# Kernel tuning notes

Hardware: AMD Instinct MI355X
Metric: run time of the kernel (lower is better)

The kernel has to match this reference:

```python
import jax, jax.numpy as jnp
import numpy as np

D_MODEL = 768
N_HEADS = 12
D_FF = 3072
D_K = D_MODEL // N_HEADS


def _layernorm(x, gamma, beta, eps=1e-5):
    mu = jnp.mean(x, axis=-1, keepdims=True)
    var = jnp.var(x, axis=-1, keepdims=True)
    return (x - mu) * jax.lax.rsqrt(var + eps) * gamma + beta


def setup_inputs() -> dict:
    key = jax.random.key(0)
    ks = jax.random.split(key, 16)
    B, S = 2, 2048
    s = 1.0 / np.sqrt(D_MODEL)
    inp = {
        "x": jax.random.normal(ks[0], (B, S, D_MODEL), jnp.float32),
        "mask": jnp.ones((B, 1, 1, S), jnp.int32),
        "wq": jax.random.normal(ks[1], (D_MODEL, D_MODEL), jnp.float32) * s,
        "bq": jnp.zeros((D_MODEL,), jnp.float32),
        "wk": jax.random.normal(ks[2], (D_MODEL, D_MODEL), jnp.float32) * s,
        "bk": jnp.zeros((D_MODEL,), jnp.float32),
        "wv": jax.random.normal(ks[3], (D_MODEL, D_MODEL), jnp.float32) * s,
        "bv": jnp.zeros((D_MODEL,), jnp.float32),
        "wo": jax.random.normal(ks[4], (D_MODEL, D_MODEL), jnp.float32) * s,
        "bo": jnp.zeros((D_MODEL,), jnp.float32),
        "w1": jax.random.normal(ks[5], (D_MODEL, D_FF), jnp.float32) * s,
        "b1": jnp.zeros((D_FF,), jnp.float32),
        "w2": jax.random.normal(ks[6], (D_FF, D_MODEL), jnp.float32) / np.sqrt(D_FF),
        "b2": jnp.zeros((D_MODEL,), jnp.float32),
        "g1": jnp.ones((D_MODEL,), jnp.float32),
        "be1": jnp.zeros((D_MODEL,), jnp.float32),
        "g2": jnp.ones((D_MODEL,), jnp.float32),
        "be2": jnp.zeros((D_MODEL,), jnp.float32),
    }
    return inp


def reference(x, mask, wq, bq, wk, bk, wv, bv, wo, bo, w1, b1, w2, b2, g1, be1, g2, be2):
    B, S, _ = x.shape
    # QKV projections, split into heads: [B, H, S, d_k]
    q = (x @ wq + bq).reshape(B, S, N_HEADS, D_K).transpose(0, 2, 1, 3)
    k = (x @ wk + bk).reshape(B, S, N_HEADS, D_K).transpose(0, 2, 1, 3)
    v = (x @ wv + bv).reshape(B, S, N_HEADS, D_K).transpose(0, 2, 1, 3)
    # [B, H, S, S]
    scores = jnp.einsum('bhqd,bhkd->bhqk', q, k) / np.sqrt(D_K).astype(np.float32)
    scores = jnp.where(mask == 0, -1e9, scores)
    attn = jax.nn.softmax(scores, axis=-1)  # dropout is identity in eval
    ctx = jnp.einsum('bhqk,bhkd->bhqd', attn, v)
    ctx = ctx.transpose(0, 2, 1, 3).reshape(B, S, D_MODEL)
    attn_out = ctx @ wo + bo
    x = _layernorm(x + attn_out, g1, be1)
    ff = jax.nn.gelu(x @ w1 + b1, approximate=False) @ w2 + b2
    x = _layernorm(x + ff, g2, be2)
    return x
```

## Files before the change

### kernel.cpp

```cpp
#include <hip/hip_runtime.h>
#include <hip/hip_bf16.h>
#include <math.h>

#define D_MODEL 768
#define N_HEADS 12
#define D_FF    3072
#define D_K     64
#define SEQ     2048
#define BATCH   2
#define M_TOK   (BATCH * SEQ)
#define D_QKV   (3 * D_MODEL)
#define BH      (BATCH * N_HEADS)

typedef __attribute__((ext_vector_type(8))) short short8;
typedef __attribute__((ext_vector_type(4))) float f32x4;

static __device__ __forceinline__ short f2bf(float f) {
    __hip_bfloat16 b = __float2bfloat16(f);
    return __builtin_bit_cast(short, b);
}

static __device__ __forceinline__ void load_lds16(const void* g, void* l) {
    __builtin_amdgcn_global_load_lds(
        (const __attribute__((address_space(1))) unsigned int*)g,
        (__attribute__((address_space(3))) unsigned int*)l,
        16, 0, 0);
}

__global__ __launch_bounds__(256) void prep_kernel(
    const float* __restrict__ x,  short* __restrict__ xb,
    const float* __restrict__ wq, const float* __restrict__ wk,
    const float* __restrict__ wv, short* __restrict__ wqkv_t,
    const float* __restrict__ wo, short* __restrict__ wo_t,
    const float* __restrict__ w1, short* __restrict__ w1_t,
    const float* __restrict__ w2, short* __restrict__ w2_t,
    const float* __restrict__ bq, const float* __restrict__ bk,
    const float* __restrict__ bv, float* __restrict__ bqkv)
{
    __shared__ float tile[32][33];
    const int bid = blockIdx.x;
    const int tid = threadIdx.x;

    if (bid < 6912) {
        const float* in; short* outp; int K, N, t;
        if (bid < 576)       { in = wq; outp = wqkv_t;                 K = 768;  N = 768;  t = bid; }
        else if (bid < 1152) { in = wk; outp = wqkv_t + 589824;        K = 768;  N = 768;  t = bid - 576; }
        else if (bid < 1728) { in = wv; outp = wqkv_t + 2 * 589824;    K = 768;  N = 768;  t = bid - 1152; }
        else if (bid < 2304) { in = wo; outp = wo_t;                   K = 768;  N = 768;  t = bid - 1728; }
        else if (bid < 4608) { in = w1; outp = w1_t;                   K = 768;  N = 3072; t = bid - 2304; }
        else                 { in = w2; outp = w2_t;                   K = 3072; N = 768;  t = bid - 4608; }
        const int nb = N >> 5;
        const int bx = t % nb, by = t / nb;
        const int n0 = bx * 32, k0 = by * 32;
        const int tx = tid & 31, ty = tid >> 5;
#pragma unroll
        for (int i = 0; i < 32; i += 8)
            tile[ty + i][tx] = in[(size_t)(k0 + ty + i) * N + n0 + tx];
        __syncthreads();
#pragma unroll
        for (int i = 0; i < 32; i += 8)
            outp[(size_t)(n0 + ty + i) * K + k0 + tx] = f2bf(tile[tx][ty + i]);
    } else if (bid < 8448) {
        const int t = (bid - 6912) * 256 + tid;
        const float4 a = reinterpret_cast<const float4*>(x)[2 * t];
        const float4 b = reinterpret_cast<const float4*>(x)[2 * t + 1];
        short8 s;
        s[0] = f2bf(a.x); s[1] = f2bf(a.y); s[2] = f2bf(a.z); s[3] = f2bf(a.w);
        s[4] = f2bf(b.x); s[5] = f2bf(b.y); s[6] = f2bf(b.z); s[7] = f2bf(b.w);
        reinterpret_cast<short8*>(xb)[t] = s;
    } else {
        const int t = (bid - 8448) * 256 + tid;
        if (t < D_QKV)
            bqkv[t] = (t < 768) ? bq[t] : (t < 1536) ? bk[t - 768] : bv[t - 1536];
    }
}

#define EPI_QKV     0
#define EPI_GELU_BF 1
#define EPI_RES_F32 2

template <int EPI>
__global__ __launch_bounds__(256) void gemm_mfma(
    const short* __restrict__ A,
    const short* __restrict__ Bt,
    const float* __restrict__ bias,
    const float* __restrict__ res,
    void* __restrict__ Cout,
    void* __restrict__ Out2,
    void* __restrict__ Out3,
    int M, int N, int K)
{
    __shared__ short As[128 * 32];
    __shared__ short Bs[128 * 32];

    const int tid  = threadIdx.x;
    const int w    = tid >> 6;
    const int lane = tid & 63;
    const int m16  = lane & 15;
    const int quad = lane >> 4;
    const int wm   = w >> 1;
    const int wn   = w & 1;
    const int bm = blockIdx.y * 128;
    const int bn = blockIdx.x * 128;

    const int sr = lane >> 2;
    const int sc = (lane & 3) * 8;

    f32x4 acc[4][4];
#pragma unroll
    for (int mt = 0; mt < 4; ++mt)
#pragma unroll
        for (int nt = 0; nt < 4; ++nt)
            acc[mt][nt] = (f32x4){0.f, 0.f, 0.f, 0.f};

    for (int k0 = 0; k0 < K; k0 += 32) {
        __syncthreads();
#pragma unroll
        for (int i = 0; i < 2; ++i) {
            const int row = i * 64 + w * 16 + sr;
            load_lds16(&A [(size_t)(bm + row) * K + k0 + sc],
                       &As[i * 2048 + w * 512]);
            load_lds16(&Bt[(size_t)(bn + row) * K + k0 + sc],
                       &Bs[i * 2048 + w * 512]);
        }
        __syncthreads();

        short8 af[4], bf[4];
#pragma unroll
        for (int mt = 0; mt < 4; ++mt)
            af[mt] = *reinterpret_cast<const short8*>(
                &As[(wm * 64 + mt * 16 + m16) * 32 + quad * 8]);
#pragma unroll
        for (int nt = 0; nt < 4; ++nt)
            bf[nt] = *reinterpret_cast<const short8*>(
                &Bs[(wn * 64 + nt * 16 + m16) * 32 + quad * 8]);
#pragma unroll
        for (int mt = 0; mt < 4; ++mt)
#pragma unroll
            for (int nt = 0; nt < 4; ++nt)
                acc[mt][nt] = __builtin_amdgcn_mfma_f32_16x16x32_bf16(
                    af[mt], bf[nt], acc[mt][nt], 0, 0, 0);
    }

#pragma unroll
    for (int mt = 0; mt < 4; ++mt) {
#pragma unroll
        for (int r = 0; r < 4; ++r) {
            const int row = bm + wm * 64 + mt * 16 + quad * 4 + r;
#pragma unroll
            for (int nt = 0; nt < 4; ++nt) {
                const int col = bn + wn * 64 + nt * 16 + m16;
                float v = acc[mt][nt][r] + bias[col];
                if (EPI == EPI_QKV) {
                    const int b = row >> 11;
                    const int s = row & 2047;
                    const int sec = (col >= 1536) ? 2 : (col >= 768) ? 1 : 0;
                    const int cm = col - sec * 768;
                    const int h = cm >> 6;
                    const int d = cm & 63;
                    const int bh = b * N_HEADS + h;
                    if (sec == 0) {
                        ((short*)Cout)[((size_t)bh * SEQ + s) * 64 + d] = f2bf(v * 0.125f);
                    } else if (sec == 1) {
                        ((short*)Out2)[((size_t)bh * SEQ + s) * 64 + d] = f2bf(v);
                    } else {
                        ((short*)Out3)[((size_t)bh * 64 + d) * SEQ + s] = f2bf(v);
                    }
                } else if (EPI == EPI_GELU_BF) {
                    v = 0.5f * v * (1.0f + erff(v * 0.70710678118654752f));
                    ((short*)Cout)[(size_t)row * N + col] = f2bf(v);
                } else {
                    v += res[(size_t)row * N + col];
                    ((float*)Cout)[(size_t)row * N + col] = v;
                }
            }
        }
    }
}

template <int EPI>
__global__ __launch_bounds__(256) void gemm_bn64(
    const short* __restrict__ A, const short* __restrict__ Bt,
    const float* __restrict__ bias, const float* __restrict__ res,
    void* __restrict__ Cout, int M, int N, int K)
{
    __shared__ short As[128 * 32];
    __shared__ short Bs[64 * 32];

    const int tid  = threadIdx.x;
    const int w    = tid >> 6;
    const int lane = tid & 63;
    const int m16  = lane & 15;
    const int quad = lane >> 4;
    const int bm = blockIdx.y * 128;
    const int bn = blockIdx.x * 64;

    const int sr = lane >> 2;
    const int sc = (lane & 3) * 8;

    f32x4 acc[2][4];
#pragma unroll
    for (int mt = 0; mt < 2; ++mt)
#pragma unroll
        for (int nt = 0; nt < 4; ++nt)
            acc[mt][nt] = (f32x4){0.f, 0.f, 0.f, 0.f};

    for (int k0 = 0; k0 < K; k0 += 32) {
        __syncthreads();
#pragma unroll
        for (int i = 0; i < 2; ++i) {
            const int row = i * 64 + w * 16 + sr;
            load_lds16(&A[(size_t)(bm + row) * K + k0 + sc],
                       &As[i * 2048 + w * 512]);
        }
        load_lds16(&Bt[(size_t)(bn + w * 16 + sr) * K + k0 + sc], &Bs[w * 512]);
        __syncthreads();

        short8 af[2], bf[4];
#pragma unroll
        for (int mt = 0; mt < 2; ++mt)
            af[mt] = *reinterpret_cast<const short8*>(
                &As[(w * 32 + mt * 16 + m16) * 32 + quad * 8]);
#pragma unroll
        for (int nt = 0; nt < 4; ++nt)
            bf[nt] = *reinterpret_cast<const short8*>(
                &Bs[(nt * 16 + m16) * 32 + quad * 8]);
#pragma unroll
        for (int mt = 0; mt < 2; ++mt)
#pragma unroll
            for (int nt = 0; nt < 4; ++nt)
                acc[mt][nt] = __builtin_amdgcn_mfma_f32_16x16x32_bf16(
                    af[mt], bf[nt], acc[mt][nt], 0, 0, 0);
    }

#pragma unroll
    for (int mt = 0; mt < 2; ++mt) {
#pragma unroll
        for (int r = 0; r < 4; ++r) {
            const int row = bm + w * 32 + mt * 16 + quad * 4 + r;
#pragma unroll
            for (int nt = 0; nt < 4; ++nt) {
                const int col = bn + nt * 16 + m16;
                float v = acc[mt][nt][r] + bias[col];
                if (EPI == EPI_RES_F32) {
                    v += res[(size_t)row * N + col];
                    ((float*)Cout)[(size_t)row * N + col] = v;
                } else {
                    ((short*)Cout)[(size_t)row * N + col] = f2bf(v);
                }
            }
        }
    }
}

#define KT 64
#define LDS_STR 72

__global__ __launch_bounds__(256) void attn_mfma_kernel(
    const short* __restrict__ qb, const short* __restrict__ kb,
    const short* __restrict__ vtb, const int* __restrict__ mask,
    short* __restrict__ ctx)
{
    __shared__ short Klds[KT * LDS_STR];
    __shared__ short Vtlds[D_K * LDS_STR];
    __shared__ short Plds[4 * 16 * LDS_STR];

    const int tid  = threadIdx.x;
    const int lane = tid & 63;
    const int wv   = tid >> 6;
    const int m16  = lane & 15;
    const int quad = lane >> 4;

    const int qtile = blockIdx.x * 64;
    const int bh = blockIdx.y;
    const int b = bh / N_HEADS;

    const size_t qrow = (size_t)bh * SEQ + qtile + wv * 16 + m16;
    short8 qf[2];
#pragma unroll
    for (int kc = 0; kc < 2; ++kc)
        qf[kc] = *reinterpret_cast<const short8*>(
            &qb[qrow * 64 + kc * 32 + quad * 8]);

    short8 ones;
#pragma unroll
    for (int i = 0; i < 8; ++i) ones[i] = (short)0x3F80;

    f32x4 o[4];
#pragma unroll
    for (int nt = 0; nt < 4; ++nt) o[nt] = (f32x4){0.f, 0.f, 0.f, 0.f};
    f32x4 lacc = (f32x4){0.f, 0.f, 0.f, 0.f};

    const int* mrow = mask + (size_t)b * SEQ;

    for (int kt0 = 0; kt0 < SEQ; kt0 += KT) {
        __syncthreads();

        {
            const int key = tid >> 2;
            const int dg = (tid & 3) * 16;
            const short* src = &kb[((size_t)bh * SEQ + kt0 + key) * 64 + dg];
            *reinterpret_cast<short8*>(&Klds[key * LDS_STR + dg]) =
                *reinterpret_cast<const short8*>(src);
            *reinterpret_cast<short8*>(&Klds[key * LDS_STR + dg + 8]) =
                *reinterpret_cast<const short8*>(src + 8);
        }
        {
            const int d = tid >> 2;
            const int kg = (tid & 3) * 16;
            const short* src = &vtb[((size_t)bh * 64 + d) * SEQ + kt0 + kg];
            *reinterpret_cast<short8*>(&Vtlds[d * LDS_STR + kg]) =
                *reinterpret_cast<const short8*>(src);
            *reinterpret_cast<short8*>(&Vtlds[d * LDS_STR + kg + 8]) =
                *reinterpret_cast<const short8*>(src + 8);
        }
        __syncthreads();

        f32x4 s[4];
#pragma unroll
        for (int nt = 0; nt < 4; ++nt) s[nt] = (f32x4){0.f, 0.f, 0.f, 0.f};
#pragma unroll
        for (int nt = 0; nt < 4; ++nt) {
#pragma unroll
            for (int kc = 0; kc < 2; ++kc) {
                const short8 kf = *reinterpret_cast<const short8*>(
                    &Klds[(nt * 16 + m16) * LDS_STR + kc * 32 + quad * 8]);
                s[nt] = __builtin_amdgcn_mfma_f32_16x16x32_bf16(qf[kc], kf, s[nt], 0, 0, 0);
            }
        }

        short* Pw = &Plds[wv * 16 * LDS_STR];
#pragma unroll
        for (int nt = 0; nt < 4; ++nt) {
            const int mk = mrow[kt0 + nt * 16 + m16];
#pragma unroll
            for (int r = 0; r < 4; ++r) {
                const float sv = (mk == 0) ? -1e9f : fminf(s[nt][r], 30.f);
                Pw[(quad * 4 + r) * LDS_STR + nt * 16 + m16] = f2bf(__expf(sv));
            }
        }

#pragma unroll
        for (int kc = 0; kc < 2; ++kc) {
            const short8 af = *reinterpret_cast<const short8*>(
                &Pw[m16 * LDS_STR + kc * 32 + quad * 8]);
#pragma unroll
            for (int nt = 0; nt < 4; ++nt) {
                const short8 bf = *reinterpret_cast<const short8*>(
                    &Vtlds[(nt * 16 + m16) * LDS_STR + kc * 32 + quad * 8]);
                o[nt] = __builtin_amdgcn_mfma_f32_16x16x32_bf16(af, bf, o[nt], 0, 0, 0);
            }
            lacc = __builtin_amdgcn_mfma_f32_16x16x32_bf16(af, ones, lacc, 0, 0, 0);
        }
    }

    const int h = bh % N_HEADS;
#pragma unroll
    for (int r = 0; r < 4; ++r) {
        const float inv_l = 1.0f / lacc[r];
        const size_t row = (size_t)(b * SEQ + qtile + wv * 16 + quad * 4 + r);
#pragma unroll
        for (int nt = 0; nt < 4; ++nt)
            ctx[row * D_MODEL + h * D_K + nt * 16 + m16] = f2bf(o[nt][r] * inv_l);
    }
}

template <bool DUAL>
__global__ __launch_bounds__(256) void layernorm_kernel(
    const float* __restrict__ in, const float* __restrict__ g,
    const float* __restrict__ be, float* __restrict__ outf,
    short* __restrict__ outb)
{
    const int row = blockIdx.x;
    const float* x = in + (size_t)row * D_MODEL;

    float s = 0.0f, s2 = 0.0f;
    for (int i = threadIdx.x; i < D_MODEL; i += 256) {
        const float v = x[i];
        s += v; s2 += v * v;
    }
#pragma unroll
    for (int off = 32; off > 0; off >>= 1) {
        s  += __shfl_down(s, off);
        s2 += __shfl_down(s2, off);
    }
    __shared__ float red[2][4];
    const int wid = threadIdx.x >> 6;
    const int lane = threadIdx.x & 63;
    if (lane == 0) { red[0][wid] = s; red[1][wid] = s2; }
    __syncthreads();
    __shared__ float stats[2];
    if (threadIdx.x == 0) {
        float ts = 0.0f, ts2 = 0.0f;
#pragma unroll
        for (int w = 0; w < 4; ++w) { ts += red[0][w]; ts2 += red[1][w]; }
        const float mu = ts * (1.0f / D_MODEL);
        const float var = ts2 * (1.0f / D_MODEL) - mu * mu;
        stats[0] = mu;
        stats[1] = rsqrtf(var + 1e-5f);
    }
    __syncthreads();
    const float mu = stats[0], rstd = stats[1];
    for (int i = threadIdx.x; i < D_MODEL; i += 256) {
        const float v = (x[i] - mu) * rstd * g[i] + be[i];
        outf[(size_t)row * D_MODEL + i] = v;
        if (DUAL) outb[(size_t)row * D_MODEL + i] = f2bf(v);
    }
}

extern "C" void kernel_launch(void* const* d_in, const int* in_sizes, int n_in,
                              void* d_out, int out_size, void* d_ws, size_t ws_size,
                              hipStream_t stream)
{
    const float* x    = (const float*)d_in[0];
    const int*   mask = (const int*)  d_in[1];
    const float* wq   = (const float*)d_in[2];
    const float* bq   = (const float*)d_in[3];
    const float* wk   = (const float*)d_in[4];
    const float* bk   = (const float*)d_in[5];
    const float* wv   = (const float*)d_in[6];
    const float* bv   = (const float*)d_in[7];
    const float* wo   = (const float*)d_in[8];
    const float* bo   = (const float*)d_in[9];
    const float* w1   = (const float*)d_in[10];
    const float* b1   = (const float*)d_in[11];
    const float* w2   = (const float*)d_in[12];
    const float* b2   = (const float*)d_in[13];
    const float* g1   = (const float*)d_in[14];
    const float* be1  = (const float*)d_in[15];
    const float* g2   = (const float*)d_in[16];
    const float* be2  = (const float*)d_in[17];

    float* out = (float*)d_out;

    char* cur = (char*)d_ws;
    auto alloc = [&](size_t bytes) { char* p = cur; cur += (bytes + 255) & ~(size_t)255; return p; };

    short* xb      = (short*)alloc((size_t)M_TOK * D_MODEL * 2);
    short* qbuf    = (short*)alloc((size_t)BH * SEQ * D_K * 2);
    short* kbuf    = (short*)alloc((size_t)BH * SEQ * D_K * 2);
    short* vtbuf   = (short*)alloc((size_t)BH * D_K * SEQ * 2);
    short* ctxb    = (short*)alloc((size_t)M_TOK * D_MODEL * 2);
    short* x1b     = (short*)alloc((size_t)M_TOK * D_MODEL * 2);
    short* ffb     = (short*)alloc((size_t)M_TOK * D_FF * 2);
    short* wqkv_t  = (short*)alloc((size_t)D_QKV * D_MODEL * 2);
    short* wo_t    = (short*)alloc((size_t)D_MODEL * D_MODEL * 2);
    short* w1_t    = (short*)alloc((size_t)D_FF * D_MODEL * 2);
    short* w2_t    = (short*)alloc((size_t)D_MODEL * D_FF * 2);
    float* bqkv    = (float*)alloc((size_t)D_QKV * 4);
    float* h1      = (float*)alloc((size_t)M_TOK * D_MODEL * 4);
    float* x1f     = (float*)alloc((size_t)M_TOK * D_MODEL * 4);
    float* h2      = (float*)alloc((size_t)M_TOK * D_MODEL * 4);

    const dim3 blk(256);

    hipLaunchKernelGGL(prep_kernel, dim3(8457), blk, 0, stream,
                       x, xb, wq, wk, wv, wqkv_t, wo, wo_t,
                       w1, w1_t, w2, w2_t, bq, bk, bv, bqkv);

    hipLaunchKernelGGL((gemm_mfma<EPI_QKV>), dim3(D_QKV / 128, M_TOK / 128), blk, 0, stream,
                       xb, wqkv_t, bqkv, nullptr, qbuf, kbuf, vtbuf, M_TOK, D_QKV, D_MODEL);

    hipLaunchKernelGGL(attn_mfma_kernel, dim3(SEQ / 64, BH), blk, 0, stream,
                       qbuf, kbuf, vtbuf, mask, ctxb);

    hipLaunchKernelGGL((gemm_bn64<EPI_RES_F32>), dim3(D_MODEL / 64, M_TOK / 128), blk, 0, stream,
                       ctxb, wo_t, bo, x, h1, M_TOK, D_MODEL, D_MODEL);

    hipLaunchKernelGGL((layernorm_kernel<true>), dim3(M_TOK), blk, 0, stream,
                       h1, g1, be1, x1f, x1b);

    hipLaunchKernelGGL((gemm_mfma<EPI_GELU_BF>), dim3(D_FF / 128, M_TOK / 128), blk, 0, stream,
                       x1b, w1_t, b1, nullptr, ffb, nullptr, nullptr, M_TOK, D_FF, D_MODEL);

    hipLaunchKernelGGL((gemm_bn64<EPI_RES_F32>), dim3(D_MODEL / 64, M_TOK / 128), blk, 0, stream,
                       ffb, w2_t, b2, x1f, h2, M_TOK, D_MODEL, D_FF);

    hipLaunchKernelGGL((layernorm_kernel<false>), dim3(M_TOK), blk, 0, stream,
                       h2, g2, be2, out, nullptr);
}
```

Before: 371.3 us.

## Deepen GEMM K-tile to 64 with XOR-swizzled LDS, widen attention key tile, approximate GELU

```diff
diff --git a/kernel.cpp b/kernel.cpp
--- a/kernel.cpp
+++ b/kernel.cpp
@@ -20,6 +20,13 @@
     return __builtin_bit_cast(short, b);
 }
 
+static __device__ __forceinline__ float gelu_f(float v) {
+    const float u = 0.7978845608f * (v + 0.044715f * v * v * v);
+    const float e = __expf(2.0f * u);
+    const float t = 1.0f - 2.0f / (e + 1.0f);
+    return 0.5f * v * (1.0f + t);
+}
+
 static __device__ __forceinline__ void load_lds16(const void* g, void* l) {
     __builtin_amdgcn_global_load_lds(
         (const __attribute__((address_space(1))) unsigned int*)g,
@@ -43,12 +50,12 @@
 
     if (bid < 6912) {
         const float* in; short* outp; int K, N, t;
-        if (bid < 576)       { in = wq; outp = wqkv_t;                 K = 768;  N = 768;  t = bid; }
-        else if (bid < 1152) { in = wk; outp = wqkv_t + 589824;        K = 768;  N = 768;  t = bid - 576; }
-        else if (bid < 1728) { in = wv; outp = wqkv_t + 2 * 589824;    K = 768;  N = 768;  t = bid - 1152; }
-        else if (bid < 2304) { in = wo; outp = wo_t;                   K = 768;  N = 768;  t = bid - 1728; }
-        else if (bid < 4608) { in = w1; outp = w1_t;                   K = 768;  N = 3072; t = bid - 2304; }
-        else                 { in = w2; outp = w2_t;                   K = 3072; N = 768;  t = bid - 4608; }
+        if (bid < 576)       { in = wq; outp = wqkv_t;              K = 768;  N = 768;  t = bid; }
+        else if (bid < 1152) { in = wk; outp = wqkv_t + 589824;     K = 768;  N = 768;  t = bid - 576; }
+        else if (bid < 1728) { in = wv; outp = wqkv_t + 2 * 589824; K = 768;  N = 768;  t = bid - 1152; }
+        else if (bid < 2304) { in = wo; outp = wo_t;                K = 768;  N = 768;  t = bid - 1728; }
+        else if (bid < 4608) { in = w1; outp = w1_t;                K = 768;  N = 3072; t = bid - 2304; }
+        else                 { in = w2; outp = w2_t;                K = 3072; N = 768;  t = bid - 4608; }
         const int nb = N >> 5;
         const int bx = t % nb, by = t / nb;
         const int n0 = bx * 32, k0 = by * 32;
@@ -85,13 +92,11 @@
     const short* __restrict__ Bt,
     const float* __restrict__ bias,
     const float* __restrict__ res,
-    void* __restrict__ Cout,
-    void* __restrict__ Out2,
-    void* __restrict__ Out3,
+    void* __restrict__ Cout, void* __restrict__ Out2, void* __restrict__ Out3,
     int M, int N, int K)
 {
-    __shared__ short As[128 * 32];
-    __shared__ short Bs[128 * 32];
+    __shared__ short As[128 * 64];
+    __shared__ short Bs[128 * 64];
 
     const int tid  = threadIdx.x;
     const int w    = tid >> 6;
@@ -103,8 +108,9 @@
     const int bm = blockIdx.y * 128;
     const int bn = blockIdx.x * 128;
 
-    const int sr = lane >> 2;
-    const int sc = (lane & 3) * 8;
+    const int l8 = lane >> 3;
+    const int scol = ((lane & 7) ^ l8) * 8;
+    const int rx = m16 & 7;
 
     f32x4 acc[4][4];
 #pragma unroll
@@ -113,33 +119,36 @@
         for (int nt = 0; nt < 4; ++nt)
             acc[mt][nt] = (f32x4){0.f, 0.f, 0.f, 0.f};
 
-    for (int k0 = 0; k0 < K; k0 += 32) {
-        __syncthreads();
-#pragma unroll
-        for (int i = 0; i < 2; ++i) {
-            const int row = i * 64 + w * 16 + sr;
-            load_lds16(&A [(size_t)(bm + row) * K + k0 + sc],
-                       &As[i * 2048 + w * 512]);
-            load_lds16(&Bt[(size_t)(bn + row) * K + k0 + sc],
-                       &Bs[i * 2048 + w * 512]);
-        }
-        __syncthreads();
-
-        short8 af[4], bf[4];
-#pragma unroll
-        for (int mt = 0; mt < 4; ++mt)
-            af[mt] = *reinterpret_cast<const short8*>(
-                &As[(wm * 64 + mt * 16 + m16) * 32 + quad * 8]);
-#pragma unroll
-        for (int nt = 0; nt < 4; ++nt)
-            bf[nt] = *reinterpret_cast<const short8*>(
-                &Bs[(wn * 64 + nt * 16 + m16) * 32 + quad * 8]);
-#pragma unroll
-        for (int mt = 0; mt < 4; ++mt)
+    for (int k0 = 0; k0 < K; k0 += 64) {
+        __syncthreads();
+#pragma unroll
+        for (int i = 0; i < 4; ++i) {
+            const int g = w * 4 + i;
+            const int row = g * 8 + l8;
+            load_lds16(&A [(size_t)(bm + row) * K + k0 + scol], &As[g * 512]);
+            load_lds16(&Bt[(size_t)(bn + row) * K + k0 + scol], &Bs[g * 512]);
+        }
+        __syncthreads();
+
+#pragma unroll
+        for (int s = 0; s < 2; ++s) {
+            const int cs = ((s * 4 + quad) ^ rx) * 8;
+            short8 af[4], bf[4];
+#pragma unroll
+            for (int mt = 0; mt < 4; ++mt)
+                af[mt] = *reinterpret_cast<const short8*>(
+                    &As[(wm * 64 + mt * 16 + m16) * 64 + cs]);
 #pragma unroll
             for (int nt = 0; nt < 4; ++nt)
-                acc[mt][nt] = __builtin_amdgcn_mfma_f32_16x16x32_bf16(
-                    af[mt], bf[nt], acc[mt][nt], 0, 0, 0);
+                bf[nt] = *reinterpret_cast<const short8*>(
+                    &Bs[(wn * 64 + nt * 16 + m16) * 64 + cs]);
+#pragma unroll
+            for (int mt = 0; mt < 4; ++mt)
+#pragma unroll
+                for (int nt = 0; nt < 4; ++nt)
+                    acc[mt][nt] = __builtin_amdgcn_mfma_f32_16x16x32_bf16(
+                        af[mt], bf[nt], acc[mt][nt], 0, 0, 0);
+        }
     }
 
 #pragma unroll
@@ -167,8 +176,7 @@
                         ((short*)Out3)[((size_t)bh * 64 + d) * SEQ + s] = f2bf(v);
                     }
                 } else if (EPI == EPI_GELU_BF) {
-                    v = 0.5f * v * (1.0f + erff(v * 0.70710678118654752f));
-                    ((short*)Cout)[(size_t)row * N + col] = f2bf(v);
+                    ((short*)Cout)[(size_t)row * N + col] = f2bf(gelu_f(v));
                 } else {
                     v += res[(size_t)row * N + col];
                     ((float*)Cout)[(size_t)row * N + col] = v;
@@ -184,8 +192,8 @@
     const float* __restrict__ bias, const float* __restrict__ res,
     void* __restrict__ Cout, int M, int N, int K)
 {
-    __shared__ short As[128 * 32];
-    __shared__ short Bs[64 * 32];
+    __shared__ short As[128 * 64];
+    __shared__ short Bs[64 * 64];
 
     const int tid  = threadIdx.x;
     const int w    = tid >> 6;
@@ -195,8 +203,9 @@
     const int bm = blockIdx.y * 128;
     const int bn = blockIdx.x * 64;
 
-    const int sr = lane >> 2;
-    const int sc = (lane & 3) * 8;
+    const int l8 = lane >> 3;
+    const int scol = ((lane & 7) ^ l8) * 8;
+    const int rx = m16 & 7;
 
     f32x4 acc[2][4];
 #pragma unroll
@@ -205,32 +214,39 @@
         for (int nt = 0; nt < 4; ++nt)
             acc[mt][nt] = (f32x4){0.f, 0.f, 0.f, 0.f};
 
-    for (int k0 = 0; k0 < K; k0 += 32) {
-        __syncthreads();
+    for (int k0 = 0; k0 < K; k0 += 64) {
+        __syncthreads();
+#pragma unroll
+        for (int i = 0; i < 4; ++i) {
+            const int g = w * 4 + i;
+            load_lds16(&A[(size_t)(bm + g * 8 + l8) * K + k0 + scol], &As[g * 512]);
+        }
 #pragma unroll
         for (int i = 0; i < 2; ++i) {
-            const int row = i * 64 + w * 16 + sr;
-            load_lds16(&A[(size_t)(bm + row) * K + k0 + sc],
-                       &As[i * 2048 + w * 512]);
-        }
-        load_lds16(&Bt[(size_t)(bn + w * 16 + sr) * K + k0 + sc], &Bs[w * 512]);
-        __syncthreads();
-
-        short8 af[2], bf[4];
-#pragma unroll
-        for (int mt = 0; mt < 2; ++mt)
-            af[mt] = *reinterpret_cast<const short8*>(
-                &As[(w * 32 + mt * 16 + m16) * 32 + quad * 8]);
-#pragma unroll
-        for (int nt = 0; nt < 4; ++nt)
-            bf[nt] = *reinterpret_cast<const short8*>(
-                &Bs[(nt * 16 + m16) * 32 + quad * 8]);
-#pragma unroll
-        for (int mt = 0; mt < 2; ++mt)
+            const int g = w * 2 + i;
+            load_lds16(&Bt[(size_t)(bn + g * 8 + l8) * K + k0 + scol], &Bs[g * 512]);
+        }
+        __syncthreads();
+
+#pragma unroll
+        for (int s = 0; s < 2; ++s) {
+            const int cs = ((s * 4 + quad) ^ rx) * 8;
+            short8 af[2], bf[4];
+#pragma unroll
+            for (int mt = 0; mt < 2; ++mt)
+                af[mt] = *reinterpret_cast<const short8*>(
+                    &As[(w * 32 + mt * 16 + m16) * 64 + cs]);
 #pragma unroll
             for (int nt = 0; nt < 4; ++nt)
-                acc[mt][nt] = __builtin_amdgcn_mfma_f32_16x16x32_bf16(
-                    af[mt], bf[nt], acc[mt][nt], 0, 0, 0);
+                bf[nt] = *reinterpret_cast<const short8*>(
+                    &Bs[(nt * 16 + m16) * 64 + cs]);
+#pragma unroll
+            for (int mt = 0; mt < 2; ++mt)
+#pragma unroll
+                for (int nt = 0; nt < 4; ++nt)
+                    acc[mt][nt] = __builtin_amdgcn_mfma_f32_16x16x32_bf16(
+                        af[mt], bf[nt], acc[mt][nt], 0, 0, 0);
+        }
     }
 
 #pragma unroll
@@ -253,17 +269,17 @@
     }
 }
 
-#define KT 64
-#define LDS_STR 72
+#define KT 128
+#define PSTR 136
 
 __global__ __launch_bounds__(256) void attn_mfma_kernel(
     const short* __restrict__ qb, const short* __restrict__ kb,
     const short* __restrict__ vtb, const int* __restrict__ mask,
     short* __restrict__ ctx)
 {
-    __shared__ short Klds[KT * LDS_STR];
-    __shared__ short Vtlds[D_K * LDS_STR];
-    __shared__ short Plds[4 * 16 * LDS_STR];
+    __shared__ short Klds[KT * 64];
+    __shared__ short Vtlds[D_K * KT];
+    __shared__ short Plds[4 * 16 * PSTR];
 
     const int tid  = threadIdx.x;
     const int lane = tid & 63;
@@ -293,61 +309,61 @@
 
     const int* mrow = mask + (size_t)b * SEQ;
 
+    const int l8 = lane >> 3;
+    const int kcol = ((lane & 7) ^ l8) * 8;
+    const int l16 = lane >> 4;
+    const int c16 = lane & 15;
+    const int rx8 = m16 & 7;
+
     for (int kt0 = 0; kt0 < SEQ; kt0 += KT) {
         __syncthreads();
-
-        {
-            const int key = tid >> 2;
-            const int dg = (tid & 3) * 16;
-            const short* src = &kb[((size_t)bh * SEQ + kt0 + key) * 64 + dg];
-            *reinterpret_cast<short8*>(&Klds[key * LDS_STR + dg]) =
-                *reinterpret_cast<const short8*>(src);
-            *reinterpret_cast<short8*>(&Klds[key * LDS_STR + dg + 8]) =
-                *reinterpret_cast<const short8*>(src + 8);
-        }
-        {
-            const int d = tid >> 2;
-            const int kg = (tid & 3) * 16;
-            const short* src = &vtb[((size_t)bh * 64 + d) * SEQ + kt0 + kg];
-            *reinterpret_cast<short8*>(&Vtlds[d * LDS_STR + kg]) =
-                *reinterpret_cast<const short8*>(src);
-            *reinterpret_cast<short8*>(&Vtlds[d * LDS_STR + kg + 8]) =
-                *reinterpret_cast<const short8*>(src + 8);
-        }
-        __syncthreads();
-
-        f32x4 s[4];
-#pragma unroll
-        for (int nt = 0; nt < 4; ++nt) s[nt] = (f32x4){0.f, 0.f, 0.f, 0.f};
-#pragma unroll
-        for (int nt = 0; nt < 4; ++nt) {
+#pragma unroll
+        for (int i = 0; i < 4; ++i) {
+            const int g = wv * 4 + i;
+            const int row = g * 8 + l8;
+            load_lds16(&kb[((size_t)bh * SEQ + kt0 + row) * 64 + kcol], &Klds[g * 512]);
+        }
+#pragma unroll
+        for (int i = 0; i < 4; ++i) {
+            const int g = wv * 4 + i;
+            const int row = g * 4 + l16;
+            const int vcol = (c16 ^ (row & 15)) * 8;
+            load_lds16(&vtb[((size_t)bh * 64 + row) * SEQ + kt0 + vcol], &Vtlds[g * 512]);
+        }
+        __syncthreads();
+
+        f32x4 s[8];
+#pragma unroll
+        for (int nt = 0; nt < 8; ++nt) s[nt] = (f32x4){0.f, 0.f, 0.f, 0.f};
+#pragma unroll
+        for (int nt = 0; nt < 8; ++nt) {
 #pragma unroll
             for (int kc = 0; kc < 2; ++kc) {
                 const short8 kf = *reinterpret_cast<const short8*>(
-                    &Klds[(nt * 16 + m16) * LDS_STR + kc * 32 + quad * 8]);
+                    &Klds[(nt * 16 + m16) * 64 + (((kc * 4 + quad) ^ rx8) * 8)]);
                 s[nt] = __builtin_amdgcn_mfma_f32_16x16x32_bf16(qf[kc], kf, s[nt], 0, 0, 0);
             }
         }
 
-        short* Pw = &Plds[wv * 16 * LDS_STR];
-#pragma unroll
-        for (int nt = 0; nt < 4; ++nt) {
+        short* Pw = &Plds[wv * 16 * PSTR];
+#pragma unroll
+        for (int nt = 0; nt < 8; ++nt) {
             const int mk = mrow[kt0 + nt * 16 + m16];
 #pragma unroll
             for (int r = 0; r < 4; ++r) {
                 const float sv = (mk == 0) ? -1e9f : fminf(s[nt][r], 30.f);
-                Pw[(quad * 4 + r) * LDS_STR + nt * 16 + m16] = f2bf(__expf(sv));
+                Pw[(quad * 4 + r) * PSTR + nt * 16 + m16] = f2bf(__expf(sv));
             }
         }
 
 #pragma unroll
-        for (int kc = 0; kc < 2; ++kc) {
+        for (int kc = 0; kc < 4; ++kc) {
             const short8 af = *reinterpret_cast<const short8*>(
-                &Pw[m16 * LDS_STR + kc * 32 + quad * 8]);
+                &Pw[m16 * PSTR + kc * 32 + quad * 8]);
 #pragma unroll
             for (int nt = 0; nt < 4; ++nt) {
                 const short8 bf = *reinterpret_cast<const short8*>(
-                    &Vtlds[(nt * 16 + m16) * LDS_STR + kc * 32 + quad * 8]);
+                    &Vtlds[(nt * 16 + m16) * KT + (((kc * 4 + quad) ^ m16) * 8)]);
                 o[nt] = __builtin_amdgcn_mfma_f32_16x16x32_bf16(af, bf, o[nt], 0, 0, 0);
             }
             lacc = __builtin_amdgcn_mfma_f32_16x16x32_bf16(af, ones, lacc, 0, 0, 0);
```

Result: faster. 320.1 us (-13.8%).
